# Kernel optimization log

Measured on AMD Instinct MI355X. Metric: run time of the kernel, lower is better.

Reference implementation:

```python
import jax, jax.numpy as jnp
import numpy as np

CEP_ORDER = 24
ALPHA = 0.42
BETA = 0.2
ONSET = 2
IR_LENGTH = 128


def _freqt_matrix(in_order, out_order, alpha):
    # diffsptk FrequencyTransform precomputed matrix A (L2, L1): c2 = c1 @ A.T
    L1, L2 = in_order + 1, out_order + 1
    A = np.zeros((L2, L1), dtype=np.float64)
    A[0, :] = alpha ** np.arange(L1)
    if L2 > 1 and L1 > 1:
        A[1, 1:] = (alpha ** np.arange(L1 - 1, dtype=np.float64)) * np.arange(1, L1) * (1.0 - alpha * alpha)
    for i in range(2, L2):
        for j in range(1, L1):
            A[i, j] = A[i - 1, j - 1] + alpha * (A[i, j - 1] - A[i - 1, j])
    return A


def _mc2b_matrix(M, alpha):
    # b[m] = mc[m] - alpha*b[m+1]  =>  b[m] = sum_{j>=m} (-alpha)^(j-m) mc[j]
    j = np.arange(M + 1)
    P = j[None, :] - j[:, None]
    return np.where(P >= 0, (-alpha) ** np.maximum(P, 0), 0.0)


def _b2mc_matrix(M, alpha):
    # mc[m] = b[m] + alpha*b[m+1]
    return np.eye(M + 1) + alpha * np.eye(M + 1, k=1)


# constants derived from hyperparameters (buffers in the torch module)
A_FT = jnp.asarray(_freqt_matrix(CEP_ORDER, IR_LENGTH - 1, -ALPHA), dtype=jnp.float32)   # (128, 25)
A_MC2B = jnp.asarray(_mc2b_matrix(CEP_ORDER, ALPHA), dtype=jnp.float32)                  # (25, 25)
A_B2MC = jnp.asarray(_b2mc_matrix(CEP_ORDER, ALPHA), dtype=jnp.float32)                  # (25, 25)
_w = np.full(CEP_ORDER + 1, 1.0 + BETA, dtype=np.float32)
_w[:ONSET] = 1.0
WEIGHT = jnp.asarray(_w)                                                                  # (25,)


def _mc2en(mc):
    # mel-cepstrum -> energy: warp to linear cepstrum (len 128), power spectrum, r[0]
    c = jnp.einsum('...m,lm->...l', mc, A_FT)                 # (..., 128)
    spec = jnp.exp(2.0 * jnp.fft.rfft(c, n=IR_LENGTH).real)   # (..., 65), real power spectrum
    # r[0] of irfft(spec): DC + Nyquist once, interior bins twice (IR_LENGTH even)
    r0 = (spec[..., 0] + spec[..., -1] + 2.0 * jnp.sum(spec[..., 1:-1], axis=-1)) / IR_LENGTH
    return r0                                                  # (...,)


def setup_inputs() -> dict:
    key = jax.random.key(0)
    mc = 0.2 * jax.random.normal(key, (16, 32768, CEP_ORDER + 1), dtype=jnp.float32)
    return {"mc": mc}


def reference(mc):
    e1 = _mc2en(mc)                                            # energy before postfilter
    mc2 = mc * WEIGHT                                          # intensity-weighted cepstrum
    e2 = _mc2en(mc2)                                           # energy after weighting
    b2 = jnp.einsum('...m,nm->...n', mc2, A_MC2B)              # mc -> MLSA coefficients
    b2 = b2.at[..., 0].add(0.5 * jnp.log(e1 / e2))             # energy compensation on b[0]
    return jnp.einsum('...m,nm->...n', b2, A_B2MC)             # MLSA -> mel-cepstrum
```

## Files before the change

### kernel.cpp

```cpp
#include <hip/hip_runtime.h>


namespace cg {

constexpr int L  = 128;
constexpr int M1 = 25;

struct CosTab { double v[L]; };
constexpr CosTab make_costab() {
    CosTab t{};
    const double PI = 3.14159265358979323846;
    for (int i = 0; i < L; ++i) {
        int j = (i <= 64) ? i : i - 128;
        double x = (2.0 * PI * (double)j) / 128.0;
        double x2 = x * x, term = 1.0, s = 1.0;
        for (int n = 1; n <= 16; ++n) {
            term *= -x2 / ((2.0 * n - 1.0) * (2.0 * n));
            s += term;
        }
        t.v[i] = s;
    }
    return t;
}
constexpr CosTab CT = make_costab();

struct AMat { double v[L][M1]; };
constexpr AMat make_aft() {
    AMat A{};
    const double al = -0.42;
    double p = 1.0;
    for (int j = 0; j < M1; ++j) { A.v[0][j] = p; p *= al; }
    double q = 1.0;
    for (int j = 1; j < M1; ++j) { A.v[1][j] = q * (double)j * (1.0 - al * al); q *= al; }
    for (int i = 2; i < L; ++i)
        for (int j = 1; j < M1; ++j)
            A.v[i][j] = A.v[i - 1][j - 1] + al * (A.v[i][j - 1] - A.v[i - 1][j]);
    return A;
}
constexpr AMat AFT = make_aft();

struct Chunk { double v[8][M1]; };
template <int K0>
constexpr Chunk make_chunk() {
    Chunk c{};
    for (int kk = 0; kk < 8; ++kk) {
        int k = K0 + kk;
        for (int m = 0; m < M1; ++m) {
            double s = 0.0;
            for (int l = 0; l < L; ++l)
                s += AFT.v[l][m] * CT.v[(k * l) & 127];
            c.v[kk][m] = s;
        }
    }
    return c;
}
constexpr Chunk CH0 = make_chunk<0>();
constexpr Chunk CH1 = make_chunk<8>();
constexpr Chunk CH2 = make_chunk<16>();
constexpr Chunk CH3 = make_chunk<24>();
constexpr Chunk CH4 = make_chunk<32>();
constexpr Chunk CH5 = make_chunk<40>();
constexpr Chunk CH6 = make_chunk<48>();
constexpr Chunk CH7 = make_chunk<56>();
constexpr Chunk CH8 = make_chunk<64>();

constexpr double chunkval(int bin, int m) {
    const Chunk* chs[9] = { &CH0, &CH1, &CH2, &CH3, &CH4, &CH5, &CH6, &CH7, &CH8 };
    return chs[bin >> 3]->v[bin & 7][m];
}

constexpr double blogical(int k, int col) {
    const double LOG2E = 1.44269504088896340736;
    if (col >= 130) return (k == 25) ? -1.0e4 : 0.0;
    int bin = (col < 65) ? col : (col - 65);
    if (k == 25) return (bin == 0 || bin == 64) ? 0.0 : 1.0;
    if (k > 25) return 0.0;
    double c = LOG2E * 2.0 * chunkval(bin, k);
    if (col >= 65 && k >= 2) c *= 1.2;
    return c;
}

constexpr unsigned short f2h(double v) {
    if (v == 0.0) return 0;
    unsigned short s = 0;
    if (v < 0) { s = 0x8000; v = -v; }
    int e = 0;
    while (v >= 2.0) { v *= 0.5; ++e; }
    while (v < 1.0)  { v *= 2.0; --e; }
    if (e > 15) return (unsigned short)(s | 0x7c00);
    if (e < -14) return s;
    int mant = (int)((v - 1.0) * 1024.0 + 0.5);
    if (mant == 1024) { mant = 0; ++e; if (e > 15) return (unsigned short)(s | 0x7c00); }
    return (unsigned short)(s | ((e + 15) << 10) | mant);
}

struct Tile { unsigned short v[64][8]; };
template <int N>
constexpr Tile make_tile() {
    Tile t{};
    for (int l = 0; l < 64; ++l)
        for (int j = 0; j < 8; ++j)
            t.v[l][j] = f2h(blogical((l >> 4) * 8 + j, N * 16 + (l & 15)));
    return t;
}
constexpr Tile T0 = make_tile<0>();
constexpr Tile T1 = make_tile<1>();
constexpr Tile T2 = make_tile<2>();
constexpr Tile T3 = make_tile<3>();
constexpr Tile T4 = make_tile<4>();
constexpr Tile T5 = make_tile<5>();
constexpr Tile T6 = make_tile<6>();
constexpr Tile T7 = make_tile<7>();
constexpr Tile T8 = make_tile<8>();

struct BH { alignas(16) unsigned short v[9][64][8]; };
constexpr BH make_bh() {
    BH b{};
    const Tile* ts[9] = { &T0, &T1, &T2, &T3, &T4, &T5, &T6, &T7, &T8 };
    for (int n = 0; n < 9; ++n)
        for (int l = 0; l < 64; ++l)
            for (int j = 0; j < 8; ++j)
                b.v[n][l][j] = ts[n]->v[l][j];
    return b;
}

}

__device__ const cg::BH g_Bh = cg::make_bh();

typedef _Float16 f16x8 __attribute__((ext_vector_type(8)));
typedef float    f32x4 __attribute__((ext_vector_type(4)));

__global__ __launch_bounds__(256, 4)
void mcpf_kernel(const float* __restrict__ mc, float* __restrict__ out) {
    __shared__ __align__(16) float sbuf[4 * 408 + 8];
    const int tid  = threadIdx.x;
    const int lane = tid & 63;
    const int wv   = tid >> 6;
    const int r0   = lane & 15;
    const int kg   = lane >> 4;

    float* __restrict__ wbuf = &sbuf[wv * 408];
    const long long gw  = (long long)blockIdx.x * 4 + wv;
    const long long b4  = gw * 100;

    const float4* __restrict__ src4  = reinterpret_cast<const float4*>(mc);
    float4*       __restrict__ dst4g = reinterpret_cast<float4*>(out);

    f16x8 bfrag[9];
#pragma unroll
    for (int n = 0; n < 9; ++n)
        bfrag[n] = *reinterpret_cast<const f16x8*>(&g_Bh.v[n][lane][0]);

    {
        const float4* __restrict__ s_ = src4 + b4;
        __builtin_amdgcn_global_load_lds(
            (const __attribute__((address_space(1))) float*)
                (const float*)(s_ + lane),
            (__attribute__((address_space(3))) float*)(wbuf),
            16, 0, 0);
        if (lane < 36)
            __builtin_amdgcn_global_load_lds(
                (const __attribute__((address_space(1))) float*)
                    (const float*)(s_ + lane + 64),
                (__attribute__((address_space(3))) float*)(wbuf + 256),
                16, 0, 0);
    }
    asm volatile("s_waitcnt vmcnt(0)" ::: "memory");

    float4* __restrict__ wb4 = reinterpret_cast<float4*>(wbuf);
    float4* __restrict__ dt4 = dst4g + b4;

    const float* __restrict__ arow = &wbuf[r0 * 25 + kg * 8];

    float tmp[8];
#pragma unroll
    for (int j = 0; j < 8; ++j) tmp[j] = arow[j];
    f16x8 af;
    af[0] = (_Float16)tmp[0];
    af[1] = (kg == 3) ? (_Float16)1.0f : (_Float16)tmp[1];
#pragma unroll
    for (int j = 2; j < 8; ++j)
        af[j] = (kg == 3) ? (_Float16)0.0f : (_Float16)tmp[j];

    float s1 = 0.0f, s2 = 0.0f;
#pragma unroll
    for (int n = 0; n < 9; ++n) {
        f32x4 acc = {0.f, 0.f, 0.f, 0.f};
        acc = __builtin_amdgcn_mfma_f32_16x16x32_f16(bfrag[n], af, acc, 0, 0, 0);
        float e0 = __builtin_amdgcn_exp2f(acc[0]);
        float e1 = __builtin_amdgcn_exp2f(acc[1]);
        float e2 = __builtin_amdgcn_exp2f(acc[2]);
        float e3 = __builtin_amdgcn_exp2f(acc[3]);
        if (n < 4) {
            s1 += (e0 + e1) + (e2 + e3);
        } else if (n == 4) {
            float h = (e0 + e1) + (e2 + e3);
            bool c = (kg == 0);
            s1 += c ? e0 : 0.0f;
            s2 += c ? (h - e0) : h;
        } else {
            s2 += (e0 + e1) + (e2 + e3);
        }
    }

    s1 += __shfl_xor(s1, 16);
    s1 += __shfl_xor(s1, 32);
    s2 += __shfl_xor(s2, 16);
    s2 += __shfl_xor(s2, 32);

    const float d = 0.34657359027997264f *
                    (__builtin_amdgcn_logf(s1) - __builtin_amdgcn_logf(s2));

#pragma unroll
    for (int j = 0; j < 2; ++j) {
        int t2 = lane + j * 64;
        if (t2 < 100) {
            float4 v = wb4[t2];
            int f = t2 * 4;
            int q = f / 25;
            int r = f - 25 * q;
            int srcl = ((r == 0) ? q : q + 1) & 15;
            float dv = __shfl(d, srcl);
            v.x *= (r     < 2)                  ? 1.0f : 1.2f;
            v.y *= (r + 1 < 2 || r + 1 == 25)   ? 1.0f : 1.2f;
            v.z *= (r + 2 == 25 || r + 2 == 26) ? 1.0f : 1.2f;
            v.w *= (r + 3 == 25 || r + 3 == 26) ? 1.0f : 1.2f;
            if (r == 0)  v.x += dv;
            if (r == 22) v.w += dv;
            if (r == 23) v.z += dv;
            if (r == 24) v.y += dv;
            dt4[t2] = v;
        }
    }
}

extern "C" void kernel_launch(void* const* d_in, const int* in_sizes, int n_in,
                              void* d_out, int out_size, void* d_ws, size_t ws_size,
                              hipStream_t stream) {
    const float* mc = (const float*)d_in[0];
    float* out = (float*)d_out;
    const int rows = in_sizes[0] / 25;
    const int blocks = rows / 64;
    mcpf_kernel<<<dim3(blocks), dim3(256), 0, stream>>>(mc, out);
}
```

Measured before the change: 24.36 us.

## Split fused kernel into energy-delta kernel and streaming apply kernel

Splits the single fused kernel in two. The first computes only the per-row energy correction d and writes it to a workspace buffer. The second is a grid-stride elementwise pass that re-reads the input, applies the weights and the correction, and writes the output. The aim is to shorten the first kernel and let the output pass stream with full occupancy, at the cost of a second launch and reading the whole input twice from memory.

After: 37.09 us. 1.52x slower.

```diff
diff --git a/kernel.cpp b/kernel.cpp
--- a/kernel.cpp
+++ b/kernel.cpp
@@ -132,7 +132,7 @@
 typedef float    f32x4 __attribute__((ext_vector_type(4)));
 
 __global__ __launch_bounds__(256, 4)
-void mcpf_kernel(const float* __restrict__ mc, float* __restrict__ out) {
+void mcpf_d(const float* __restrict__ mc, float* __restrict__ dbuf) {
     __shared__ __align__(16) float sbuf[4 * 408 + 8];
     const int tid  = threadIdx.x;
     const int lane = tid & 63;
@@ -144,8 +144,7 @@
     const long long gw  = (long long)blockIdx.x * 4 + wv;
     const long long b4  = gw * 100;
 
-    const float4* __restrict__ src4  = reinterpret_cast<const float4*>(mc);
-    float4*       __restrict__ dst4g = reinterpret_cast<float4*>(out);
+    const float4* __restrict__ src4 = reinterpret_cast<const float4*>(mc);
 
     f16x8 bfrag[9];
 #pragma unroll
@@ -167,9 +166,6 @@
                 16, 0, 0);
     }
     asm volatile("s_waitcnt vmcnt(0)" ::: "memory");
-
-    float4* __restrict__ wb4 = reinterpret_cast<float4*>(wbuf);
-    float4* __restrict__ dt4 = dst4g + b4;
 
     const float* __restrict__ arow = &wbuf[r0 * 25 + kg * 8];
 
@@ -212,26 +208,31 @@
     const float d = 0.34657359027997264f *
                     (__builtin_amdgcn_logf(s1) - __builtin_amdgcn_logf(s2));
 
-#pragma unroll
-    for (int j = 0; j < 2; ++j) {
-        int t2 = lane + j * 64;
-        if (t2 < 100) {
-            float4 v = wb4[t2];
-            int f = t2 * 4;
-            int q = f / 25;
-            int r = f - 25 * q;
-            int srcl = ((r == 0) ? q : q + 1) & 15;
-            float dv = __shfl(d, srcl);
-            v.x *= (r     < 2)                  ? 1.0f : 1.2f;
-            v.y *= (r + 1 < 2 || r + 1 == 25)   ? 1.0f : 1.2f;
-            v.z *= (r + 2 == 25 || r + 2 == 26) ? 1.0f : 1.2f;
-            v.w *= (r + 3 == 25 || r + 3 == 26) ? 1.0f : 1.2f;
-            if (r == 0)  v.x += dv;
-            if (r == 22) v.w += dv;
-            if (r == 23) v.z += dv;
-            if (r == 24) v.y += dv;
-            dt4[t2] = v;
-        }
+    if (kg == 0) dbuf[gw * 16 + r0] = d;
+}
+
+__global__ __launch_bounds__(256)
+void mcpf_apply(const float* __restrict__ mc, const float* __restrict__ dbuf,
+                float* __restrict__ out, int nf4) {
+    const float4* __restrict__ src4 = reinterpret_cast<const float4*>(mc);
+    float4* __restrict__ dst4 = reinterpret_cast<float4*>(out);
+    const int stride = gridDim.x * 256;
+    for (int idx = blockIdx.x * 256 + threadIdx.x; idx < nf4; idx += stride) {
+        float4 v = src4[idx];
+        int f = idx * 4;
+        int q = f / 25;
+        int r = f - 25 * q;
+        float dv0 = dbuf[q];
+        float dv1 = dbuf[q + 1];
+        v.x *= (r     < 2)                  ? 1.0f : 1.2f;
+        v.y *= (r + 1 < 2 || r + 1 == 25)   ? 1.0f : 1.2f;
+        v.z *= (r + 2 == 25 || r + 2 == 26) ? 1.0f : 1.2f;
+        v.w *= (r + 3 == 25 || r + 3 == 26) ? 1.0f : 1.2f;
+        if (r == 0)  v.x += dv0;
+        if (r == 22) v.w += dv1;
+        if (r == 23) v.z += dv1;
+        if (r == 24) v.y += dv1;
+        dst4[idx] = v;
     }
 }
 
@@ -240,7 +241,9 @@
                               hipStream_t stream) {
     const float* mc = (const float*)d_in[0];
     float* out = (float*)d_out;
+    float* dbuf = (float*)d_ws;
     const int rows = in_sizes[0] / 25;
-    const int blocks = rows / 64;
-    mcpf_kernel<<<dim3(blocks), dim3(256), 0, stream>>>(mc, out);
-}
+    const int nf4  = in_sizes[0] / 4;
+    mcpf_d<<<dim3(rows / 64), dim3(256), 0, stream>>>(mc, dbuf);
+    mcpf_apply<<<dim3(2048), dim3(256), 0, stream>>>(mc, dbuf, out, nf4);
+}
```
